# Performance work log

Measured on AMD Instinct MI355X. Metric: run time of the kernel, lower is better.

The kernel has to match this reference:

```python
import jax, jax.numpy as jnp
import numpy as np

B, N, IN_DIM, DIM, H, TOPK = 2, 2048, 256, 256, 8, 4
DH = DIM // H  # 32
EPS = 1e-5


def setup_inputs() -> dict:
    key = jax.random.key(0)
    ks = jax.random.split(key, 6)
    points = jax.random.normal(ks[0], (B * N, IN_DIM), dtype=jnp.float32)
    norm_gamma = jnp.ones((IN_DIM,), dtype=jnp.float32)
    norm_beta = jnp.zeros((IN_DIM,), dtype=jnp.float32)
    w_qkv = jax.random.normal(ks[1], (3 * DIM, IN_DIM), dtype=jnp.float32) / np.sqrt(IN_DIM)
    w_proj = jax.random.normal(ks[2], (DIM, DIM), dtype=jnp.float32) / np.sqrt(DIM)
    b_proj = jnp.zeros((DIM,), dtype=jnp.float32)
    return {"points": points, "norm_gamma": norm_gamma, "norm_beta": norm_beta,
            "w_qkv": w_qkv, "w_proj": w_proj, "b_proj": b_proj}


def reference(points, norm_gamma, norm_beta, w_qkv, w_proj, b_proj):
    # norm1 (LayerNorm over channel)
    x = points.reshape(B, N, IN_DIM)
    mu = jnp.mean(x, axis=-1, keepdims=True)
    var = jnp.var(x, axis=-1, keepdims=True)
    x = (x - mu) / jnp.sqrt(var + EPS) * norm_gamma + norm_beta
    # fused qkv: [B,N,3,H,DH]
    qkv = (x @ w_qkv.T).reshape(B, N, 3, H, DH)
    q, k, v = qkv[:, :, 0], qkv[:, :, 1], qkv[:, :, 2]  # [B,N,H,DH]
    # dense coarse attention: QK [B, M(query), S(key), H]
    qk = jnp.einsum('blhd,bshd->blsh', q, k)
    temp = 1.0 / np.sqrt(DH)
    A = jax.nn.softmax(temp * qk, axis=2)  # softmax over keys (dim=-2)
    # topk over key axis; zero out the top-k entries (scatter mask of zeros)
    A_t = jnp.transpose(A, (0, 1, 3, 2))  # [B,M,H,S]
    topk_score, topk_idx = jax.lax.top_k(A_t, TOPK)  # [B,M,H,k]
    bb = jnp.arange(B)[:, None, None, None]
    mm = jnp.arange(N)[None, :, None, None]
    hh = jnp.arange(H)[None, None, :, None]
    mask_t = jnp.ones_like(A_t).at[bb, mm, hh, topk_idx].set(0.0)
    # message = (A * mask) @ V
    message = jnp.einsum('blhs,bshd->blhd', A_t * mask_t, v).reshape(B, N, DIM)
    message = message @ w_proj.T + b_proj
    v_flat = v.reshape(B, N, DIM)
    message = v_flat + message
    # no padding (equal slens), so ~padding_mask selects everything -> flatten
    message_flat = message.reshape(B * N, DIM)
    topk_score_flat = jnp.transpose(topk_score, (0, 1, 3, 2)).reshape(B * N, TOPK, H)
    topk_idx_flat = jnp.transpose(topk_idx, (0, 1, 3, 2)).reshape(B * N, TOPK, H)
    return message_flat, topk_score_flat, topk_idx_flat
```

## Files before the change

kernel.cpp:

```cpp
#include <hip/hip_runtime.h>
#include <math.h>

#define B_ 2
#define N_ 2048
#define IN_DIM_ 256
#define DIM_ 256
#define H_ 8
#define DH_ 32
#define TOPK_ 4
#define EPS_ 1e-5f
#define TEMP_ 0.17677669529663687f

__global__ __launch_bounds__(256) void ln_kernel(const float* __restrict__ x,
                                                 const float* __restrict__ gamma,
                                                 const float* __restrict__ beta,
                                                 float* __restrict__ xn) {
  int w = threadIdx.x >> 6, ld = threadIdx.x & 63;
  int row = blockIdx.x * 4 + w;
  const float4* xr = (const float4*)(x + (size_t)row * 256);
  float4 v = xr[ld];
  float s = v.x + v.y + v.z + v.w;
  float ss = v.x * v.x + v.y * v.y + v.z * v.z + v.w * v.w;
  #pragma unroll
  for (int off = 1; off < 64; off <<= 1) {
    s += __shfl_xor(s, off);
    ss += __shfl_xor(ss, off);
  }
  float mu = s * (1.0f / 256.0f);
  float var = ss * (1.0f / 256.0f) - mu * mu;
  float rstd = rsqrtf(var + EPS_);
  float4 g = ((const float4*)gamma)[ld];
  float4 bt = ((const float4*)beta)[ld];
  float4 o;
  o.x = (v.x - mu) * rstd * g.x + bt.x;
  o.y = (v.y - mu) * rstd * g.y + bt.y;
  o.z = (v.z - mu) * rstd * g.z + bt.z;
  o.w = (v.w - mu) * rstd * g.w + bt.w;
  ((float4*)(xn + (size_t)row * 256))[ld] = o;
}

template <bool PROJ>
__global__ __launch_bounds__(256) void gemm_nt(const float* __restrict__ A,
                                               const float* __restrict__ Bm,
                                               float* __restrict__ C,
                                               const float* __restrict__ vres,
                                               const float* __restrict__ bias,
                                               int K, int ldc) {
  __shared__ float As[32][64];
  __shared__ float Bs[32][64];
  int m0 = blockIdx.x * 64, n0 = blockIdx.y * 64;
  int t = threadIdx.x;
  int tm = t & 15, tn = t >> 4;
  float acc[4][4] = {};
  for (int k0 = 0; k0 < K; k0 += 32) {
    __syncthreads();
    for (int f = t; f < 512; f += 256) {
      int row = f >> 3, j = f & 7;
      float4 a = *(const float4*)(A + (size_t)(m0 + row) * K + k0 + j * 4);
      As[j * 4 + 0][row] = a.x; As[j * 4 + 1][row] = a.y;
      As[j * 4 + 2][row] = a.z; As[j * 4 + 3][row] = a.w;
      float4 b = *(const float4*)(Bm + (size_t)(n0 + row) * K + k0 + j * 4);
      Bs[j * 4 + 0][row] = b.x; Bs[j * 4 + 1][row] = b.y;
      Bs[j * 4 + 2][row] = b.z; Bs[j * 4 + 3][row] = b.w;
    }
    __syncthreads();
    #pragma unroll
    for (int k = 0; k < 32; k++) {
      float4 a = *(const float4*)&As[k][tm * 4];
      float4 b = *(const float4*)&Bs[k][tn * 4];
      float av[4] = {a.x, a.y, a.z, a.w};
      float bv[4] = {b.x, b.y, b.z, b.w};
      #pragma unroll
      for (int i = 0; i < 4; i++)
        #pragma unroll
        for (int j = 0; j < 4; j++)
          acc[i][j] = fmaf(av[i], bv[j], acc[i][j]);
    }
  }
  #pragma unroll
  for (int i = 0; i < 4; i++) {
    int m = m0 + tm * 4 + i;
    int n = n0 + tn * 4;
    float4 r = {acc[i][0], acc[i][1], acc[i][2], acc[i][3]};
    if (PROJ) {
      float4 vr = *(const float4*)(vres + (size_t)m * 768 + n);
      float4 bb = *(const float4*)(bias + n);
      r.x += vr.x + bb.x; r.y += vr.y + bb.y;
      r.z += vr.z + bb.z; r.w += vr.w + bb.w;
    }
    *(float4*)(C + (size_t)m * ldc + n) = r;
  }
}


__global__ __launch_bounds__(512, 2) void attn_kernel(const float* __restrict__ qkv,
                                                      float* __restrict__ msg,
                                                      float* __restrict__ out_s,
                                                      float* __restrict__ out_i) {
  const int l0 = blockIdx.x * 64;
  const int h = blockIdx.y;
  const int b = blockIdx.z;
  const int t = threadIdx.x;
  const int wid = __builtin_amdgcn_readfirstlane(t >> 6);
  const int lane = t & 63;
  const int c0 = wid * 8;

  __shared__ float Pm[8][64];
  __shared__ float Pl[8][64];
  __shared__ float Ptv[8][64][5];
  __shared__ int   Pti[8][64][5];
  __shared__ float AccO[64][33];
  __shared__ float Fsc[64][4];
  __shared__ int   Ffi[64][4];
  __shared__ float Flinv[64];

  const float* qrow = qkv + ((size_t)(b * N_) + l0 + lane) * 768 + h * DH_;
  float4 q[8];
  #pragma unroll
  for (int j = 0; j < 8; j++) {
    float4 v = ((const float4*)qrow)[j];
    v.x *= TEMP_; v.y *= TEMP_; v.z *= TEMP_; v.w *= TEMP_;
    q[j] = v;
  }

  float4 o[8];
  #pragma unroll
  for (int j = 0; j < 8; j++) o[j] = make_float4(0.f, 0.f, 0.f, 0.f);
  float m = -INFINITY, l = 0.f;
  float tv[4];
  int ti[4];
  #pragma unroll
  for (int i = 0; i < 4; i++) { tv[i] = -INFINITY; ti[i] = 0x7fffffff; }

  const float* Kg = qkv + (size_t)(b * N_) * 768 + 256 + h * DH_;
  const float* Vg = Kg + 256;

  #pragma unroll 1
  for (int t0 = 0; t0 < N_ / 64; ++t0) {
    const int s0 = t0 * 64;
    const float* kb = Kg + (size_t)(s0 + c0) * 768;

    float sv[8];
    #pragma unroll
    for (int c = 0; c < 8; ++c) {
      const float* kc = kb + (size_t)c * 768;
      float4 a = {0.f, 0.f, 0.f, 0.f};
      #pragma unroll
      for (int d = 0; d < 8; ++d) {
        float4 kv = *(const float4*)(kc + d * 4);
        float4 qv = q[d];
        a.x = fmaf(qv.x, kv.x, a.x);
        a.y = fmaf(qv.y, kv.y, a.y);
        a.z = fmaf(qv.z, kv.z, a.z);
        a.w = fmaf(qv.w, kv.w, a.w);
      }
      sv[c] = (a.x + a.y) + (a.z + a.w);
    }

    #pragma unroll
    for (int i = 0; i < 8; ++i) {
      float sval = sv[i];
      int idx = s0 + c0 + i;
      if (sval > tv[3] || (sval == tv[3] && idx < ti[3])) {
        bool i2 = (sval > tv[2]) || (sval == tv[2] && idx < ti[2]);
        bool i1 = (sval > tv[1]) || (sval == tv[1] && idx < ti[1]);
        bool i0 = (sval > tv[0]) || (sval == tv[0] && idx < ti[0]);
        tv[3] = i2 ? tv[2] : sval; ti[3] = i2 ? ti[2] : idx;
        float nv2 = i1 ? tv[1] : sval; int ni2 = i1 ? ti[1] : idx;
        float nv1 = i0 ? tv[0] : sval; int ni1 = i0 ? ti[0] : idx;
        if (i2) { tv[2] = nv2; ti[2] = ni2; }
        if (i1) { tv[1] = nv1; ti[1] = ni1; }
        if (i0) { tv[0] = sval; ti[0] = idx; }
      }
    }

    float tmax = fmaxf(fmaxf(fmaxf(sv[0], sv[1]), fmaxf(sv[2], sv[3])),
                       fmaxf(fmaxf(sv[4], sv[5]), fmaxf(sv[6], sv[7])));
    float mnew = fmaxf(m, tmax);
    float alpha = __expf(m - mnew);
    float ps = 0.f;
    #pragma unroll
    for (int i = 0; i < 8; ++i) { sv[i] = __expf(sv[i] - mnew); ps += sv[i]; }
    l = l * alpha + ps;
    m = mnew;
    #pragma unroll
    for (int ch = 0; ch < 8; ++ch) {
      o[ch].x *= alpha; o[ch].y *= alpha; o[ch].z *= alpha; o[ch].w *= alpha;
    }

    #pragma unroll
    for (int c = 0; c < 8; ++c) {
      float pc = sv[c];
      const float* vc = Vg + (size_t)(s0 + c0 + c) * 768;
      #pragma unroll
      for (int ch = 0; ch < 8; ++ch) {
        float4 vv = *(const float4*)(vc + ch * 4);
        o[ch].x = fmaf(pc, vv.x, o[ch].x);
        o[ch].y = fmaf(pc, vv.y, o[ch].y);
        o[ch].z = fmaf(pc, vv.z, o[ch].z);
        o[ch].w = fmaf(pc, vv.w, o[ch].w);
      }
    }
  }

  Pm[wid][lane] = m;
  Pl[wid][lane] = l;
  #pragma unroll
  for (int i = 0; i < 4; ++i) { Ptv[wid][lane][i] = tv[i]; Pti[wid][lane][i] = ti[i]; }
  for (int i = t; i < 64 * 33; i += 512) (&AccO[0][0])[i] = 0.f;
  __syncthreads();

  float mg = Pm[0][lane];
  #pragma unroll
  for (int j = 1; j < 8; ++j) mg = fmaxf(mg, Pm[j][lane]);
  float lg = 0.f;
  #pragma unroll
  for (int j = 0; j < 8; ++j) lg += Pl[j][lane] * __expf(Pm[j][lane] - mg);
  float aw = __expf(m - mg);
  #pragma unroll
  for (int ch = 0; ch < 8; ++ch) {
    atomicAdd(&AccO[lane][ch * 4 + 0], o[ch].x * aw);
    atomicAdd(&AccO[lane][ch * 4 + 1], o[ch].y * aw);
    atomicAdd(&AccO[lane][ch * 4 + 2], o[ch].z * aw);
    atomicAdd(&AccO[lane][ch * 4 + 3], o[ch].w * aw);
  }
  __syncthreads();

  if (wid == 0) {
    float linv = 1.f / lg;
    Flinv[lane] = linv;
    float fv[4];
    int fi[4];
    #pragma unroll
    for (int r = 0; r < 4; ++r) {
      float best = -INFINITY;
      int bi = 0x7fffffff, bj = 0, bii = 0;
      #pragma unroll
      for (int j = 0; j < 8; ++j)
        #pragma unroll
        for (int i2 = 0; i2 < 4; ++i2) {
          float v2 = Ptv[j][lane][i2];
          int ix = Pti[j][lane][i2];
          if (v2 > best || (v2 == best && ix < bi)) { best = v2; bi = ix; bj = j; bii = i2; }
        }
      Ptv[bj][lane][bii] = -INFINITY;
      fv[r] = best;
      fi[r] = bi;
    }
    size_t base = ((size_t)(b * N_) + l0 + lane) * TOPK_;
    #pragma unroll
    for (int r = 0; r < 4; ++r) {
      float sc = __expf(fv[r] - mg) * linv;
      Fsc[lane][r] = sc;
      Ffi[lane][r] = fi[r];
      out_s[(base + r) * H_ + h] = sc;
      out_i[(base + r) * H_ + h] = (float)fi[r];
    }
  }
  __syncthreads();

  {
    int r = t >> 3, dc = t & 7;
    float linv = Flinv[r];
    float ax = AccO[r][dc * 4 + 0] * linv;
    float ay = AccO[r][dc * 4 + 1] * linv;
    float az = AccO[r][dc * 4 + 2] * linv;
    float aw2 = AccO[r][dc * 4 + 3] * linv;
    #pragma unroll
    for (int k = 0; k < 4; ++k) {
      int idx = Ffi[r][k];
      float sc = Fsc[r][k];
      const float* vp = qkv + ((size_t)(b * N_) + idx) * 768 + 512 + h * DH_ + dc * 4;
      float4 vv = *(const float4*)vp;
      ax = fmaf(-sc, vv.x, ax); ay = fmaf(-sc, vv.y, ay);
      az = fmaf(-sc, vv.z, az); aw2 = fmaf(-sc, vv.w, aw2);
    }
    float4 r4 = {ax, ay, az, aw2};
    *(float4*)(msg + ((size_t)(b * N_) + l0 + r) * DIM_ + h * DH_ + dc * 4) = r4;
  }
}

extern "C" void kernel_launch(void* const* d_in, const int* in_sizes, int n_in,
                              void* d_out, int out_size, void* d_ws, size_t ws_size,
                              hipStream_t stream) {
  const float* points = (const float*)d_in[0];
  const float* norm_gamma = (const float*)d_in[1];
  const float* norm_beta = (const float*)d_in[2];
  const float* w_qkv = (const float*)d_in[3];
  const float* w_proj = (const float*)d_in[4];
  const float* b_proj = (const float*)d_in[5];

  float* out0 = (float*)d_out;
  float* out1 = out0 + (size_t)4096 * 256;
  float* out2 = out1 + (size_t)4096 * 4 * 8;

  float* xn = (float*)d_ws;
  float* qkv = xn + (size_t)4096 * 256;
  float* msg = qkv + (size_t)4096 * 768;

  ln_kernel<<<1024, 256, 0, stream>>>(points, norm_gamma, norm_beta, xn);
  gemm_nt<false><<<dim3(64, 12), 256, 0, stream>>>(xn, w_qkv, qkv, nullptr,
                                                   nullptr, 256, 768);
  attn_kernel<<<dim3(N_ / 64, H_, B_), 512, 0, stream>>>(qkv, msg, out1, out2);
  gemm_nt<true><<<dim3(64, 4), 256, 0, stream>>>(msg, w_proj, out0, qkv + 512,
                                                 b_proj, 256, 256);
}
```

Before: 444.9 us.

## Split attention over key halves with atomic merge and drop running-max softmax

Attention is split into two key-range halves per query tile, doubling the block count. Partial outputs and softmax denominators are accumulated with global atomics, and a separate merge kernel combines the per-half top-k candidates, normalizes, and subtracts the top-k contributions. The online-softmax running max and rescaling are removed, so exp is applied to raw scores. This saves per-tile work but can overflow for large logits. It also adds a memset, global atomics and an extra kernel launch.

```diff
diff --git a/kernel.cpp b/kernel.cpp
--- a/kernel.cpp
+++ b/kernel.cpp
@@ -93,26 +93,24 @@
 }
 
 
-__global__ __launch_bounds__(512, 2) void attn_kernel(const float* __restrict__ qkv,
-                                                      float* __restrict__ msg,
-                                                      float* __restrict__ out_s,
-                                                      float* __restrict__ out_i) {
-  const int l0 = blockIdx.x * 64;
+__global__ __launch_bounds__(512, 4) void attn_part(const float* __restrict__ qkv,
+                                                    float* __restrict__ omsg,
+                                                    float* __restrict__ lbuf,
+                                                    float* __restrict__ t4v,
+                                                    int* __restrict__ t4i) {
+  const int tile = blockIdx.x;
   const int h = blockIdx.y;
-  const int b = blockIdx.z;
+  const int b = blockIdx.z >> 1, half = blockIdx.z & 1;
+  const int l0 = tile * 64;
   const int t = threadIdx.x;
   const int wid = __builtin_amdgcn_readfirstlane(t >> 6);
   const int lane = t & 63;
   const int c0 = wid * 8;
 
-  __shared__ float Pm[8][64];
+  __shared__ float AccO[64][33];
   __shared__ float Pl[8][64];
-  __shared__ float Ptv[8][64][5];
-  __shared__ int   Pti[8][64][5];
-  __shared__ float AccO[64][33];
-  __shared__ float Fsc[64][4];
-  __shared__ int   Ffi[64][4];
-  __shared__ float Flinv[64];
+  __shared__ float Ptv[8][64][4];
+  __shared__ int   Pti[8][64][4];
 
   const float* qrow = qkv + ((size_t)(b * N_) + l0 + lane) * 768 + h * DH_;
   float4 q[8];
@@ -126,7 +124,7 @@
   float4 o[8];
   #pragma unroll
   for (int j = 0; j < 8; j++) o[j] = make_float4(0.f, 0.f, 0.f, 0.f);
-  float m = -INFINITY, l = 0.f;
+  float l = 0.f;
   float tv[4];
   int ti[4];
   #pragma unroll
@@ -134,10 +132,11 @@
 
   const float* Kg = qkv + (size_t)(b * N_) * 768 + 256 + h * DH_;
   const float* Vg = Kg + 256;
+  const int sbase = half * (N_ / 2);
 
   #pragma unroll 1
-  for (int t0 = 0; t0 < N_ / 64; ++t0) {
-    const int s0 = t0 * 64;
+  for (int t0 = 0; t0 < N_ / 128; ++t0) {
+    const int s0 = sbase + t0 * 64;
     const float* kb = Kg + (size_t)(s0 + c0) * 768;
 
     float sv[8];
@@ -174,19 +173,10 @@
       }
     }
 
-    float tmax = fmaxf(fmaxf(fmaxf(sv[0], sv[1]), fmaxf(sv[2], sv[3])),
-                       fmaxf(fmaxf(sv[4], sv[5]), fmaxf(sv[6], sv[7])));
-    float mnew = fmaxf(m, tmax);
-    float alpha = __expf(m - mnew);
     float ps = 0.f;
     #pragma unroll
-    for (int i = 0; i < 8; ++i) { sv[i] = __expf(sv[i] - mnew); ps += sv[i]; }
-    l = l * alpha + ps;
-    m = mnew;
-    #pragma unroll
-    for (int ch = 0; ch < 8; ++ch) {
-      o[ch].x *= alpha; o[ch].y *= alpha; o[ch].z *= alpha; o[ch].w *= alpha;
-    }
+    for (int i = 0; i < 8; ++i) { sv[i] = __expf(sv[i]); ps += sv[i]; }
+    l += ps;
 
     #pragma unroll
     for (int c = 0; c < 8; ++c) {
@@ -203,34 +193,27 @@
     }
   }
 
-  Pm[wid][lane] = m;
   Pl[wid][lane] = l;
   #pragma unroll
   for (int i = 0; i < 4; ++i) { Ptv[wid][lane][i] = tv[i]; Pti[wid][lane][i] = ti[i]; }
   for (int i = t; i < 64 * 33; i += 512) (&AccO[0][0])[i] = 0.f;
   __syncthreads();
 
-  float mg = Pm[0][lane];
-  #pragma unroll
-  for (int j = 1; j < 8; ++j) mg = fmaxf(mg, Pm[j][lane]);
-  float lg = 0.f;
-  #pragma unroll
-  for (int j = 0; j < 8; ++j) lg += Pl[j][lane] * __expf(Pm[j][lane] - mg);
-  float aw = __expf(m - mg);
   #pragma unroll
   for (int ch = 0; ch < 8; ++ch) {
-    atomicAdd(&AccO[lane][ch * 4 + 0], o[ch].x * aw);
-    atomicAdd(&AccO[lane][ch * 4 + 1], o[ch].y * aw);
-    atomicAdd(&AccO[lane][ch * 4 + 2], o[ch].z * aw);
-    atomicAdd(&AccO[lane][ch * 4 + 3], o[ch].w * aw);
+    atomicAdd(&AccO[lane][ch * 4 + 0], o[ch].x);
+    atomicAdd(&AccO[lane][ch * 4 + 1], o[ch].y);
+    atomicAdd(&AccO[lane][ch * 4 + 2], o[ch].z);
+    atomicAdd(&AccO[lane][ch * 4 + 3], o[ch].w);
   }
   __syncthreads();
 
   if (wid == 0) {
-    float linv = 1.f / lg;
-    Flinv[lane] = linv;
-    float fv[4];
-    int fi[4];
+    float lg = 0.f;
+    #pragma unroll
+    for (int j = 0; j < 8; ++j) lg += Pl[j][lane];
+    int e = (b * N_ + l0 + lane) * H_ + h;
+    atomicAdd(&lbuf[e], lg);
     #pragma unroll
     for (int r = 0; r < 4; ++r) {
       float best = -INFINITY;
@@ -244,39 +227,84 @@
           if (v2 > best || (v2 == best && ix < bi)) { best = v2; bi = ix; bj = j; bii = i2; }
         }
       Ptv[bj][lane][bii] = -INFINITY;
-      fv[r] = best;
-      fi[r] = bi;
-    }
-    size_t base = ((size_t)(b * N_) + l0 + lane) * TOPK_;
-    #pragma unroll
-    for (int r = 0; r < 4; ++r) {
-      float sc = __expf(fv[r] - mg) * linv;
-      Fsc[lane][r] = sc;
-      Ffi[lane][r] = fi[r];
-      out_s[(base + r) * H_ + h] = sc;
-      out_i[(base + r) * H_ + h] = (float)fi[r];
-    }
-  }
-  __syncthreads();
+      t4v[((size_t)e * 2 + half) * 4 + r] = best;
+      t4i[((size_t)e * 2 + half) * 4 + r] = bi;
+    }
+  }
 
   {
     int r = t >> 3, dc = t & 7;
-    float linv = Flinv[r];
-    float ax = AccO[r][dc * 4 + 0] * linv;
-    float ay = AccO[r][dc * 4 + 1] * linv;
-    float az = AccO[r][dc * 4 + 2] * linv;
-    float aw2 = AccO[r][dc * 4 + 3] * linv;
-    #pragma unroll
-    for (int k = 0; k < 4; ++k) {
-      int idx = Ffi[r][k];
-      float sc = Fsc[r][k];
-      const float* vp = qkv + ((size_t)(b * N_) + idx) * 768 + 512 + h * DH_ + dc * 4;
-      float4 vv = *(const float4*)vp;
-      ax = fmaf(-sc, vv.x, ax); ay = fmaf(-sc, vv.y, ay);
-      az = fmaf(-sc, vv.z, az); aw2 = fmaf(-sc, vv.w, aw2);
-    }
-    float4 r4 = {ax, ay, az, aw2};
-    *(float4*)(msg + ((size_t)(b * N_) + l0 + r) * DIM_ + h * DH_ + dc * 4) = r4;
+    float* mp = omsg + ((size_t)(b * N_) + l0 + r) * DIM_ + h * DH_ + dc * 4;
+    atomicAdd(mp + 0, AccO[r][dc * 4 + 0]);
+    atomicAdd(mp + 1, AccO[r][dc * 4 + 1]);
+    atomicAdd(mp + 2, AccO[r][dc * 4 + 2]);
+    atomicAdd(mp + 3, AccO[r][dc * 4 + 3]);
+  }
+}
+
+__global__ __launch_bounds__(256) void attn_merge(const float* __restrict__ qkv,
+                                                  float* __restrict__ omsg,
+                                                  const float* __restrict__ lbuf,
+                                                  const float* __restrict__ t4v,
+                                                  const int* __restrict__ t4i,
+                                                  float* __restrict__ out_s,
+                                                  float* __restrict__ out_i) {
+  int g = blockIdx.x * 256 + threadIdx.x;
+  int e = g >> 3, dc = g & 7;
+  int h = e & 7;
+  int prow = e >> 3;
+  int b = prow >> 11;
+
+  float linv = 1.0f / lbuf[e];
+
+  float cv[8];
+  int ci[8];
+  #pragma unroll
+  for (int c = 0; c < 8; ++c) {
+    cv[c] = t4v[(size_t)e * 8 + c];
+    ci[c] = t4i[(size_t)e * 8 + c];
+  }
+  float fv[4];
+  int fi[4];
+  unsigned used = 0;
+  #pragma unroll
+  for (int r = 0; r < 4; ++r) {
+    float best = -INFINITY;
+    int bi = 0x7fffffff, bp = 0;
+    #pragma unroll
+    for (int c = 0; c < 8; ++c) {
+      bool ok = !((used >> c) & 1);
+      if (ok && (cv[c] > best || (cv[c] == best && ci[c] < bi))) {
+        best = cv[c]; bi = ci[c]; bp = c;
+      }
+    }
+    used |= (1u << bp);
+    fv[r] = best;
+    fi[r] = bi;
+  }
+  float sc[4];
+  #pragma unroll
+  for (int r = 0; r < 4; ++r) sc[r] = __expf(fv[r]) * linv;
+
+  float* mp = omsg + (size_t)prow * DIM_ + h * DH_ + dc * 4;
+  float4 o = *(const float4*)mp;
+  o.x *= linv; o.y *= linv; o.z *= linv; o.w *= linv;
+  #pragma unroll
+  for (int r = 0; r < 4; ++r) {
+    const float* vp = qkv + ((size_t)(b * N_) + fi[r]) * 768 + 512 + h * DH_ + dc * 4;
+    float4 vv = *(const float4*)vp;
+    o.x = fmaf(-sc[r], vv.x, o.x); o.y = fmaf(-sc[r], vv.y, o.y);
+    o.z = fmaf(-sc[r], vv.z, o.z); o.w = fmaf(-sc[r], vv.w, o.w);
+  }
+  *(float4*)mp = o;
+
+  if (dc == 0) {
+    size_t base = (size_t)prow * TOPK_;
+    #pragma unroll
+    for (int r = 0; r < 4; ++r) {
+      out_s[(base + r) * H_ + h] = sc[r];
+      out_i[(base + r) * H_ + h] = (float)fi[r];
+    }
   }
 }
 
@@ -297,11 +325,16 @@
   float* xn = (float*)d_ws;
   float* qkv = xn + (size_t)4096 * 256;
   float* msg = qkv + (size_t)4096 * 768;
+  float* lbuf = msg + (size_t)4096 * 256;
+  float* t4v = xn;
+  int* t4i = (int*)(xn + 262144);
 
   ln_kernel<<<1024, 256, 0, stream>>>(points, norm_gamma, norm_beta, xn);
   gemm_nt<false><<<dim3(64, 12), 256, 0, stream>>>(xn, w_qkv, qkv, nullptr,
                                                    nullptr, 256, 768);
-  attn_kernel<<<dim3(N_ / 64, H_, B_), 512, 0, stream>>>(qkv, msg, out1, out2);
+  hipMemsetAsync(msg, 0, ((size_t)4096 * 256 + 32768) * sizeof(float), stream);
+  attn_part<<<dim3(N_ / 64, H_, B_ * 2), 512, 0, stream>>>(qkv, msg, lbuf, t4v, t4i);
+  attn_merge<<<1024, 256, 0, stream>>>(qkv, msg, lbuf, t4v, t4i, out1, out2);
   gemm_nt<true><<<dim3(64, 4), 256, 0, stream>>>(msg, w_proj, out0, qkv + 512,
                                                  b_proj, 256, 256);
 }
```

Result: slower. 462.5 us (+4.0%).
